# Kernel tuning notes

Hardware: AMD Instinct MI355X
Metric: run time of the kernel (lower is better)

Reference implementation:

```python
import jax, jax.numpy as jnp
import numpy as np

N, E, IN, H, OUT = 100000, 1600000, 64, 64, 10
NEG_SLOPE = 0.2  # PyG GATConv default negative_slope


def _glorot(key, shape):
    fan = sum(shape) if len(shape) > 1 else shape[0]
    return jax.random.normal(key, shape, dtype=jnp.float32) * jnp.sqrt(2.0 / fan)


def setup_inputs() -> dict:
    key = jax.random.key(0)
    ks = jax.random.split(key, 16)
    x = jax.random.normal(ks[0], (N, IN), dtype=jnp.float32)
    edge_index = jax.random.randint(ks[1], (2, E), 0, N, dtype=jnp.int32)
    dims = [(IN, H), (H, H), (H, OUT)]
    params = {}
    for i, (fi, fo) in enumerate(dims, start=1):
        params[f"W{i}"] = _glorot(ks[4 * i - 2], (fi, fo))
        params[f"a{i}s"] = _glorot(ks[4 * i - 1], (fo,))
        params[f"a{i}d"] = _glorot(ks[4 * i], (fo,))
        params[f"b{i}"] = jnp.zeros((fo,), dtype=jnp.float32)
    return {"x": x, "edge_index": edge_index, **params}


def gat_conv(x, src, dst, W, a_s, a_d, b):
    """Single-head GATConv (PyG defaults): gather -> leaky_relu scores ->
    segment softmax over dst -> scatter-add aggregate."""
    n = x.shape[0]
    h = x @ W                                   # [N, Fo]
    alpha_src = h @ a_s                          # [N]
    alpha_dst = h @ a_d                          # [N]
    e = jax.nn.leaky_relu(alpha_src[src] + alpha_dst[dst], NEG_SLOPE)  # [E']
    m = jax.ops.segment_max(e, dst, num_segments=n)                    # stable softmax max
    ex = jnp.exp(e - m[dst])
    denom = jax.ops.segment_sum(ex, dst, num_segments=n)
    alpha = ex / denom[dst]                      # [E'] per-dst softmax
    out = jax.ops.segment_sum(alpha[:, None] * h[src], dst, num_segments=n)
    return out + b


def reference(x, edge_index, W1, a1s, a1d, b1, W2, a2s, a2d, b2, W3, a3s, a3d, b3):
    n = x.shape[0]
    loops = jnp.arange(n, dtype=edge_index.dtype)  # add_self_loops=True
    src = jnp.concatenate([edge_index[0], loops])
    dst = jnp.concatenate([edge_index[1], loops])
    h = jax.nn.relu(gat_conv(x, src, dst, W1, a1s, a1d, b1))
    # dropout is identity at inference (training=False)
    h = jax.nn.relu(gat_conv(h, src, dst, W2, a2s, a2d, b2))
    h = gat_conv(h, src, dst, W3, a3s, a3d, b3)
    return jax.nn.log_softmax(h, axis=1)
```

## Files before the change

### kernel.cpp

```cpp
#include <hip/hip_runtime.h>
#include <math.h>
#include <type_traits>


#define NEG_SLOPE 0.2f
#define BKT_BITS 9
#define BKT_SZ   512
#define PACK_SRC_BITS 20

typedef _Float16 h8v __attribute__((ext_vector_type(8)));
typedef _Float16 h4v __attribute__((ext_vector_type(4)));
typedef float f4v __attribute__((ext_vector_type(4)));

__global__ __launch_bounds__(512) void k_bscan(const int* __restrict__ bcount, int nb,
                                               int E, int N, int* __restrict__ ebase,
                                               int* __restrict__ gcur,
                                               int* __restrict__ rowptr) {
    __shared__ int sm[BKT_SZ];
    int t = threadIdx.x;
    int v = (t < nb) ? bcount[t] : 0;
    sm[t] = v;
    __syncthreads();
    for (int o = 1; o < BKT_SZ; o <<= 1) {
        int tv = (t >= o) ? sm[t - o] : 0;
        __syncthreads();
        sm[t] += tv;
        __syncthreads();
    }
    int excl = sm[t] - v;
    if (t < nb) {
        ebase[t] = excl;
        gcur[t] = excl;
    }
    if (t == nb - 1) ebase[nb] = excl + v;
    if (t == 0) rowptr[N] = E + N;
}

__global__ __launch_bounds__(1024) void k_bscatter(const int* __restrict__ src,
                                                   const int* __restrict__ dst, int E,
                                                   int nb, int* __restrict__ gcur,
                                                   int* __restrict__ ebuf) {
    __shared__ int lc[BKT_SZ];
    __shared__ int gb[BKT_SZ];
    for (int i = threadIdx.x; i < nb; i += 1024) lc[i] = 0;
    __syncthreads();
    int base = blockIdx.x * 8192;
    int bkt[8], rnk[8], pk[8];
#pragma unroll
    for (int j = 0; j < 8; j++) {
        int i = base + j * 1024 + threadIdx.x;
        bkt[j] = -1;
        if (i < E) {
            int d = dst[i];
            int s = src[i];
            int b = d >> BKT_BITS;
            bkt[j] = b;
            rnk[j] = atomicAdd(&lc[b], 1);
            pk[j] = ((d & (BKT_SZ - 1)) << PACK_SRC_BITS) | s;
        }
    }
    __syncthreads();
    for (int b = threadIdx.x; b < nb; b += 1024)
        if (lc[b]) gb[b] = atomicAdd(&gcur[b], lc[b]);
    __syncthreads();
#pragma unroll
    for (int j = 0; j < 8; j++)
        if (bkt[j] >= 0) ebuf[gb[bkt[j]] + rnk[j]] = pk[j];
}

__global__ __launch_bounds__(512) void k_bcsr(const int* __restrict__ ebuf,
                                              const int* __restrict__ ebase, int N,
                                              int* __restrict__ rowptr,
                                              int* __restrict__ csr) {
    __shared__ int cnt[BKT_SZ];
    __shared__ int sm[BKT_SZ];
    int b = blockIdx.x;
    int t = threadIdx.x;
    int n0 = b << BKT_BITS;
    int nn = min(BKT_SZ, N - n0);
    cnt[t] = 0;
    __syncthreads();
    int e0 = ebase[b], e1 = ebase[b + 1];
    for (int i = e0 + t; i < e1; i += BKT_SZ)
        atomicAdd(&cnt[ebuf[i] >> PACK_SRC_BITS], 1);
    __syncthreads();
    int v = cnt[t] + (t < nn ? 1 : 0);
    sm[t] = v;
    __syncthreads();
    for (int o = 1; o < BKT_SZ; o <<= 1) {
        int tv = (t >= o) ? sm[t - o] : 0;
        __syncthreads();
        sm[t] += tv;
        __syncthreads();
    }
    int excl = sm[t] - v;
    int cb = e0 + n0;
    if (t < nn) {
        rowptr[n0 + t] = cb + excl;
        csr[cb + excl] = n0 + t;
    }
    cnt[t] = excl + 1;
    __syncthreads();
    for (int i = e0 + t; i < e1; i += BKT_SZ) {
        int p = ebuf[i];
        int dl = p >> PACK_SRC_BITS;
        int pos = atomicAdd(&cnt[dl], 1);
        csr[cb + pos] = p & ((1 << PACK_SRC_BITS) - 1);
    }
}

__global__ __launch_bounds__(256) void k_fill(const int* __restrict__ csr,
                                              const float* __restrict__ asb,
                                              int Etot, float* __restrict__ asbE) {
    int tid = blockIdx.x * 256 + threadIdx.x;
    int nth = gridDim.x * 256;
    int i = tid;
    for (; i + 3 * nth < Etot; i += 4 * nth) {
        int s0 = csr[i];
        int s1 = csr[i + nth];
        int s2 = csr[i + 2 * nth];
        int s3 = csr[i + 3 * nth];
        float v0 = asb[s0];
        float v1 = asb[s1];
        float v2 = asb[s2];
        float v3 = asb[s3];
        asbE[i] = v0;
        asbE[i + nth] = v1;
        asbE[i + 2 * nth] = v2;
        asbE[i + 3 * nth] = v3;
    }
    for (; i < Etot; i += nth) asbE[i] = asb[csr[i]];
}

__device__ __forceinline__ void gemm64_body(
    int bid, int nblocks, const float* __restrict__ X, const float* __restrict__ W,
    const float* __restrict__ a_s, const float* __restrict__ a_d, int N,
    _Float16* __restrict__ H, float* __restrict__ asb, float* __restrict__ adb) {
    constexpr int NT = 4;
    int lane = threadIdx.x & 63;
    int quad = lane >> 4;
    int c16 = lane & 15;

    h8v bf[NT][2];
    float asv[NT], adv[NT];
#pragma unroll
    for (int nt = 0; nt < NT; nt++) {
        int n = nt * 16 + c16;
        asv[nt] = a_s[n];
        adv[nt] = a_d[n];
#pragma unroll
        for (int kt = 0; kt < 2; kt++)
#pragma unroll
            for (int j = 0; j < 8; j++) {
                int k = kt * 32 + quad * 8 + j;
                bf[nt][kt][j] = (_Float16)W[k * 64 + n];
            }
    }

    int wid = (bid * 256 + (int)threadIdx.x) >> 6;
    int nw = (nblocks * 256) >> 6;
    int ntile = (N + 15) >> 4;

    for (int t = wid; t < ntile; t += nw) {
        int m0 = t << 4;
        int row = m0 + c16;
        const float* xr = X + (size_t)min(row, N - 1) * 64;
        h8v af[2];
#pragma unroll
        for (int kt = 0; kt < 2; kt++) {
            f4v x0 = *(const f4v*)(xr + kt * 32 + quad * 8);
            f4v x1 = *(const f4v*)(xr + kt * 32 + quad * 8 + 4);
#pragma unroll
            for (int j = 0; j < 4; j++) {
                af[kt][j] = (_Float16)x0[j];
                af[kt][4 + j] = (_Float16)x1[j];
            }
        }
        f4v c[NT];
#pragma unroll
        for (int nt = 0; nt < NT; nt++) c[nt] = (f4v){0.f, 0.f, 0.f, 0.f};
#pragma unroll
        for (int kt = 0; kt < 2; kt++)
#pragma unroll
            for (int nt = 0; nt < NT; nt++)
                c[nt] = __builtin_amdgcn_mfma_f32_16x16x32_f16(af[kt], bf[nt][kt],
                                                               c[nt], 0, 0, 0);
#pragma unroll
        for (int reg = 0; reg < 4; reg++) {
            int r = m0 + quad * 4 + reg;
            if (r < N) {
#pragma unroll
                for (int nt = 0; nt < NT; nt++)
                    H[(size_t)r * 64 + nt * 16 + c16] = (_Float16)c[nt][reg];
            }
        }
        float ps[4], pd[4];
#pragma unroll
        for (int reg = 0; reg < 4; reg++) {
            ps[reg] = 0.f;
            pd[reg] = 0.f;
#pragma unroll
            for (int nt = 0; nt < NT; nt++) {
                ps[reg] = fmaf(c[nt][reg], asv[nt], ps[reg]);
                pd[reg] = fmaf(c[nt][reg], adv[nt], pd[reg]);
            }
        }
        for (int o = 1; o < 16; o <<= 1) {
#pragma unroll
            for (int reg = 0; reg < 4; reg++) {
                ps[reg] += __shfl_xor(ps[reg], o, 64);
                pd[reg] += __shfl_xor(pd[reg], o, 64);
            }
        }
        if (c16 == 0) {
#pragma unroll
            for (int reg = 0; reg < 4; reg++) {
                int r = m0 + quad * 4 + reg;
                if (r < N) {
                    asb[r] = ps[reg];
                    adb[r] = pd[reg];
                }
            }
        }
    }
}

__global__ __launch_bounds__(256) void k_hist_gemm(
    const int* __restrict__ dst, int E, int nb, int* __restrict__ bcount,
    int histBlocks,
    const float* __restrict__ X, const float* __restrict__ W,
    const float* __restrict__ a_s, const float* __restrict__ a_d, int N,
    _Float16* __restrict__ H, float* __restrict__ asb, float* __restrict__ adb) {
    __shared__ int h[BKT_SZ];
    int bid = blockIdx.x;
    if (bid < histBlocks) {
        for (int i = threadIdx.x; i < nb; i += 256) h[i] = 0;
        __syncthreads();
        for (int i = bid * 256 + threadIdx.x; i < E; i += histBlocks * 256)
            atomicAdd(&h[dst[i] >> BKT_BITS], 1);
        __syncthreads();
        for (int i = threadIdx.x; i < nb; i += 256)
            if (h[i]) atomicAdd(&bcount[i], h[i]);
    } else {
        gemm64_body(bid - histBlocks, (int)gridDim.x - histBlocks, X, W, a_s, a_d,
                    N, H, asb, adb);
    }
}

template <int FP, typename InT>
__global__ __launch_bounds__(256) void k_gemm(
    const InT* __restrict__ X, const float* __restrict__ W,
    const float* __restrict__ a_s, const float* __restrict__ a_d,
    int N, int Freal,
    _Float16* __restrict__ H, float* __restrict__ asb, float* __restrict__ adb) {
    constexpr int NT = FP / 16;
    int lane = threadIdx.x & 63;
    int quad = lane >> 4;
    int c16 = lane & 15;

    h8v bf[NT][2];
    float asv[NT], adv[NT];
#pragma unroll
    for (int nt = 0; nt < NT; nt++) {
        int n = nt * 16 + c16;
        bool ok = (n < Freal);
        asv[nt] = ok ? a_s[n] : 0.f;
        adv[nt] = ok ? a_d[n] : 0.f;
#pragma unroll
        for (int kt = 0; kt < 2; kt++)
#pragma unroll
            for (int j = 0; j < 8; j++) {
                int k = kt * 32 + quad * 8 + j;
                bf[nt][kt][j] = (_Float16)(ok ? W[k * Freal + n] : 0.f);
            }
    }

    int wid = (blockIdx.x * blockDim.x + threadIdx.x) >> 6;
    int nw = (gridDim.x * blockDim.x) >> 6;
    int ntile = (N + 15) >> 4;

    for (int t = wid; t < ntile; t += nw) {
        int m0 = t << 4;
        int row = m0 + c16;
        const InT* xr = X + (size_t)min(row, N - 1) * 64;
        h8v af[2];
        if constexpr (std::is_same<InT, float>::value) {
#pragma unroll
            for (int kt = 0; kt < 2; kt++) {
                f4v x0 = *(const f4v*)(xr + kt * 32 + quad * 8);
                f4v x1 = *(const f4v*)(xr + kt * 32 + quad * 8 + 4);
#pragma unroll
                for (int j = 0; j < 4; j++) {
                    af[kt][j] = (_Float16)x0[j];
                    af[kt][4 + j] = (_Float16)x1[j];
                }
            }
        } else {
#pragma unroll
            for (int kt = 0; kt < 2; kt++)
                af[kt] = *(const h8v*)(xr + kt * 32 + quad * 8);
        }
        f4v c[NT];
#pragma unroll
        for (int nt = 0; nt < NT; nt++) c[nt] = (f4v){0.f, 0.f, 0.f, 0.f};
#pragma unroll
        for (int kt = 0; kt < 2; kt++)
#pragma unroll
            for (int nt = 0; nt < NT; nt++)
                c[nt] = __builtin_amdgcn_mfma_f32_16x16x32_f16(af[kt], bf[nt][kt],
                                                               c[nt], 0, 0, 0);
#pragma unroll
        for (int reg = 0; reg < 4; reg++) {
            int r = m0 + quad * 4 + reg;
            if (r < N) {
#pragma unroll
                for (int nt = 0; nt < NT; nt++)
                    H[(size_t)r * FP + nt * 16 + c16] = (_Float16)c[nt][reg];
            }
        }
        float ps[4], pd[4];
#pragma unroll
        for (int reg = 0; reg < 4; reg++) {
            ps[reg] = 0.f;
            pd[reg] = 0.f;
#pragma unroll
            for (int nt = 0; nt < NT; nt++) {
                ps[reg] = fmaf(c[nt][reg], asv[nt], ps[reg]);
                pd[reg] = fmaf(c[nt][reg], adv[nt], pd[reg]);
            }
        }
        for (int o = 1; o < 16; o <<= 1) {
#pragma unroll
            for (int reg = 0; reg < 4; reg++) {
                ps[reg] += __shfl_xor(ps[reg], o, 64);
                pd[reg] += __shfl_xor(pd[reg], o, 64);
            }
        }
        if (c16 == 0) {
#pragma unroll
            for (int reg = 0; reg < 4; reg++) {
                int r = m0 + quad * 4 + reg;
                if (r < N) {
                    asb[r] = ps[reg];
                    adb[r] = pd[reg];
                }
            }
        }
    }
}

template <int FP>
__device__ __forceinline__ void agg_slow(
    int node, const _Float16* __restrict__ H, const float* __restrict__ asbE,
    const float* __restrict__ adb, const float* __restrict__ bias,
    const int* __restrict__ rowptr, const int* __restrict__ csr,
    int N, int Freal, void* __restrict__ out, int mode, int lane) {
    if (node >= N) return;
    int start = rowptr[node];
    int end = rowptr[node + 1];
    float ad = adb[node];
    int lf = lane & (FP - 1);
    const float NEG_INF = -__builtin_inff();

    float m = NEG_INF;
    for (int base = start; base < end; base += 64) {
        int i = base + lane;
        if (i < end) {
            float t = asbE[i] + ad;
            float e = (t > 0.f) ? t : NEG_SLOPE * t;
            m = fmaxf(m, e);
        }
    }
    for (int o = 32; o > 0; o >>= 1) m = fmaxf(m, __shfl_xor(m, o, 64));
    float dsum = 0.f, acc = 0.f;
    for (int base = start; base < end; base += 64) {
        int i = base + lane;
        int cnt = min(64, end - base);
        int s = 0;
        float p = 0.f;
        if (i < end) {
            s = csr[i];
            float t = asbE[i] + ad;
            float e = (t > 0.f) ? t : NEG_SLOPE * t;
            p = __expf(e - m);
        }
        dsum += p;
        for (int j = 0; j < cnt; j++) {
            float pj = __shfl(p, j, 64);
            int sj = __shfl(s, j, 64);
            acc = fmaf(pj, (float)H[(size_t)sj * FP + lf], acc);
        }
    }
    for (int o = 32; o > 0; o >>= 1) dsum += __shfl_xor(dsum, o, 64);

    float b = (lf < Freal) ? bias[lf] : 0.f;
    float z = acc / dsum + b;
    if (mode == 0) {
        if (lane < FP)
            ((_Float16*)out)[(size_t)node * FP + lane] = (_Float16)fmaxf(z, 0.f);
    } else {
        float zz = (lane < Freal) ? z : NEG_INF;
        float zm = zz;
        for (int o = 32; o > 0; o >>= 1) zm = fmaxf(zm, __shfl_xor(zm, o, 64));
        float ez = (lane < Freal) ? __expf(zz - zm) : 0.f;
        float es = ez;
        for (int o = 32; o > 0; o >>= 1) es += __shfl_xor(es, o, 64);
        if (lane < Freal)
            ((float*)out)[(size_t)node * Freal + lane] = zz - zm - __logf(es);
    }
}

template <int FP, int W>
__global__ __launch_bounds__(256) void k_agg(
    const _Float16* __restrict__ H, const float* __restrict__ asbE,
    const float* __restrict__ adb, const float* __restrict__ bias,
    const int* __restrict__ rowptr, const int* __restrict__ csr,
    int N, int Freal, void* __restrict__ out, int mode) {
    constexpr int LPR = FP / W;
    constexpr int GRPH = 32 / LPR;
    constexpr int MAXIT = 32 / GRPH;
    using vecW = typename std::conditional<W == 8, h8v, h4v>::type;
    int lane = threadIdx.x & 63;
    int half = lane >> 5;
    int li = lane & 31;
    int wid = (blockIdx.x * blockDim.x + threadIdx.x) >> 6;
    int nA = 2 * wid;
    if (nA >= N) return;
    int n = nA + half;
    bool valid = (n < N);
    int start = 0, end = 0;
    float ad = 0.f;
    if (valid) {
        start = rowptr[n];
        end = rowptr[n + 1];
        ad = adb[n];
    }
    int deg = end - start;
    int degm = max(deg, __shfl_xor(deg, 32, 64));

    const float NEG_INF = -__builtin_inff();

    if (degm <= 32) {
        int g = li / LPR;
        int fl = li % LPR;
        bool have = (li < deg);
        int s = 0;
        float as_v = 0.f;
        if (have) {
            s = csr[start + li];
            as_v = asbE[start + li];
        }

        vecW r[MAXIT];
        int gidx = half * 32 + g;
#pragma unroll
        for (int it = 0; it < MAXIT; ++it) {
            if (it * GRPH < degm) {
                int sj = __shfl(s, gidx + it * GRPH, 64);
                r[it] = ((const vecW*)(H + (size_t)sj * FP))[fl];
            }
        }

        float e = NEG_INF;
        if (have) {
            float t = as_v + ad;
            e = (t > 0.f) ? t : NEG_SLOPE * t;
        }
        float m = e;
        for (int o = 16; o > 0; o >>= 1) m = fmaxf(m, __shfl_xor(m, o, 64));
        float p = have ? __expf(e - m) : 0.f;

        float acc[W];
#pragma unroll
        for (int c = 0; c < W; c++) acc[c] = 0.f;
#pragma unroll
        for (int it = 0; it < MAXIT; ++it) {
            if (it * GRPH < degm) {
                float pj = __shfl(p, gidx + it * GRPH, 64);
#pragma unroll
                for (int c = 0; c < W; c++)
                    acc[c] = fmaf(pj, (float)r[it][c], acc[c]);
            }
        }

        float dsum = p;
        for (int o = 16; o > 0; o >>= 1) dsum += __shfl_xor(dsum, o, 64);

        for (int o = LPR; o < 32; o <<= 1) {
#pragma unroll
            for (int c = 0; c < W; c++) acc[c] += __shfl_xor(acc[c], o, 64);
        }
        float inv = 1.f / dsum;
        int fbase = fl * W;

        if (mode == 0) {
            if (valid && li < LPR) {
                vecW zh;
#pragma unroll
                for (int c = 0; c < W; c++)
                    zh[c] = (_Float16)fmaxf(fmaf(acc[c], inv, bias[fbase + c]), 0.f);
                ((vecW*)((_Float16*)out + (size_t)n * FP))[fl] = zh;
            }
        } else {
            float zc[W];
#pragma unroll
            for (int c = 0; c < W; c++) {
                int f = fbase + c;
                zc[c] = (f < Freal) ? fmaf(acc[c], inv, bias[f]) : NEG_INF;
            }
            float vm = zc[0];
#pragma unroll
            for (int c = 1; c < W; c++) vm = fmaxf(vm, zc[c]);
            for (int o = 1; o < LPR; o <<= 1) vm = fmaxf(vm, __shfl_xor(vm, o, 64));
            float es = 0.f;
#pragma unroll
            for (int c = 0; c < W; c++) es += __expf(zc[c] - vm);
            for (int o = 1; o < LPR; o <<= 1) es += __shfl_xor(es, o, 64);
            float ls = __logf(es);
            if (valid && li < LPR) {
#pragma unroll
                for (int c = 0; c < W; c++) {
                    int f = fbase + c;
                    if (f < Freal)
                        ((float*)out)[(size_t)n * Freal + f] = zc[c] - vm - ls;
                }
            }
        }
    } else {
        agg_slow<FP>(nA, H, asbE, adb, bias, rowptr, csr, N, Freal, out, mode, lane);
        agg_slow<FP>(nA + 1, H, asbE, adb, bias, rowptr, csr, N, Freal, out, mode, lane);
    }
}

extern "C" void kernel_launch(void* const* d_in, const int* in_sizes, int n_in,
                              void* d_out, int out_size, void* d_ws, size_t ws_size,
                              hipStream_t stream) {
    const float* x = (const float*)d_in[0];
    const int* ei = (const int*)d_in[1];
    const float* W1 = (const float*)d_in[2];
    const float* a1s = (const float*)d_in[3];
    const float* a1d = (const float*)d_in[4];
    const float* b1 = (const float*)d_in[5];
    const float* W2 = (const float*)d_in[6];
    const float* a2s = (const float*)d_in[7];
    const float* a2d = (const float*)d_in[8];
    const float* b2 = (const float*)d_in[9];
    const float* W3 = (const float*)d_in[10];
    const float* a3s = (const float*)d_in[11];
    const float* a3d = (const float*)d_in[12];
    const float* b3 = (const float*)d_in[13];

    const int N = in_sizes[0] / 64;
    const int E = in_sizes[1] / 2;
    const int Etot = E + N;
    const int nb = (N + BKT_SZ - 1) >> BKT_BITS;
    const int* srcv = ei;
    const int* dstv = ei + E;

    size_t off = 0;
    char* base = (char*)d_ws;
    auto carve = [&](size_t bytes) -> void* {
        void* p = base + off;
        off = (off + bytes + 255) & ~(size_t)255;
        return p;
    };
    int* bcount = (int*)carve((size_t)(nb + 1) * 4);
    int* ebase = (int*)carve((size_t)(nb + 1) * 4);
    int* gcur = (int*)carve((size_t)nb * 4);
    int* rowptr = (int*)carve((size_t)(N + 1) * 4);
    int* csr = (int*)carve((size_t)Etot * 4);
    float* asb = (float*)carve((size_t)N * 4);
    float* adb = (float*)carve((size_t)N * 4);
    float* asbE = (float*)carve((size_t)Etot * 4);
    _Float16* hA = (_Float16*)carve((size_t)N * 64 * 2);
    _Float16* fB = (_Float16*)carve((size_t)N * 64 * 2);
    _Float16* hC = (_Float16*)carve((size_t)N * 16 * 2);
    int* ebuf = (int*)carve((size_t)E * 4);

    const int aggBlocks = (N + 7) / 8;
    const int gemmBlocks = 784;
    const int histBlocks = 512;
    const int fillBlocks = 1024;

    hipMemsetAsync(bcount, 0, (size_t)nb * 4, stream);
    k_hist_gemm<<<histBlocks + gemmBlocks, 256, 0, stream>>>(
        dstv, E, nb, bcount, histBlocks, x, W1, a1s, a1d, N, hA, asb, adb);
    k_bscan<<<1, BKT_SZ, 0, stream>>>(bcount, nb, E, N, ebase, gcur, rowptr);
    k_bscatter<<<(E + 8191) / 8192, 1024, 0, stream>>>(srcv, dstv, E, nb, gcur, ebuf);
    k_bcsr<<<nb, BKT_SZ, 0, stream>>>(ebuf, ebase, N, rowptr, csr);

    k_fill<<<fillBlocks, 256, 0, stream>>>(csr, asb, Etot, asbE);
    k_agg<64, 8><<<aggBlocks, 256, 0, stream>>>(hA, asbE, adb, b1, rowptr, csr, N, 64,
                                                (void*)fB, 0);
    k_gemm<64, _Float16><<<gemmBlocks, 256, 0, stream>>>(fB, W2, a2s, a2d, N, 64, hA,
                                                         asb, adb);
    k_fill<<<fillBlocks, 256, 0, stream>>>(csr, asb, Etot, asbE);
    k_agg<64, 8><<<aggBlocks, 256, 0, stream>>>(hA, asbE, adb, b2, rowptr, csr, N, 64,
                                                (void*)fB, 0);
    k_gemm<16, _Float16><<<gemmBlocks, 256, 0, stream>>>(fB, W3, a3s, a3d, N, 10, hC,
                                                         asb, adb);
    k_fill<<<fillBlocks, 256, 0, stream>>>(csr, asb, Etot, asbE);
    k_agg<16, 4><<<aggBlocks, 256, 0, stream>>>(hC, asbE, adb, b3, rowptr, csr, N, 10,
                                                d_out, 1);
}
```

Measured before the change: 332.2 us.

## Fold attention projections into aggregation epilogue and fuse fill with GEMM/CSR build

Precomputes W·a_s and W·a_d for layers 2 and 3 so the next layer's per-node attention logits come straight from the aggregation output, which removes that reduction from the GEMM. The layer-1 source-score gather now happens while the CSR is built, which drops one fill kernel. The other fills run as extra blocks inside the GEMM launch so both share one grid. This cuts three launches and overlaps a gather-bound pass with MFMA work, at the cost of extra shuffles in the aggregation epilogue and slightly different rounding, since the logits are computed from the fp32 pre-GEMM activations.

```diff
diff --git a/kernel.cpp b/kernel.cpp
--- a/kernel.cpp
+++ b/kernel.cpp
@@ -12,12 +12,34 @@
 typedef _Float16 h4v __attribute__((ext_vector_type(4)));
 typedef float f4v __attribute__((ext_vector_type(4)));
 
-__global__ __launch_bounds__(512) void k_bscan(const int* __restrict__ bcount, int nb,
-                                               int E, int N, int* __restrict__ ebase,
-                                               int* __restrict__ gcur,
-                                               int* __restrict__ rowptr) {
+__global__ __launch_bounds__(512) void k_bscan(
+    const int* __restrict__ bcount, int nb, int E, int N,
+    int* __restrict__ ebase, int* __restrict__ gcur, int* __restrict__ rowptr,
+    const float* __restrict__ W2, const float* __restrict__ a2s,
+    const float* __restrict__ a2d, const float* __restrict__ W3,
+    const float* __restrict__ a3s, const float* __restrict__ a3d,
+    float* __restrict__ w2s, float* __restrict__ w2d,
+    float* __restrict__ w3s, float* __restrict__ w3d) {
     __shared__ int sm[BKT_SZ];
     int t = threadIdx.x;
+
+    if (t < 64) {
+        float s2 = 0.f, d2 = 0.f;
+        for (int k = 0; k < 64; k++) {
+            s2 = fmaf(W2[t * 64 + k], a2s[k], s2);
+            d2 = fmaf(W2[t * 64 + k], a2d[k], d2);
+        }
+        w2s[t] = s2;
+        w2d[t] = d2;
+        float s3 = 0.f, d3 = 0.f;
+        for (int k = 0; k < 10; k++) {
+            s3 = fmaf(W3[t * 10 + k], a3s[k], s3);
+            d3 = fmaf(W3[t * 10 + k], a3d[k], d3);
+        }
+        w3s[t] = s3;
+        w3d[t] = d3;
+    }
+
     int v = (t < nb) ? bcount[t] : 0;
     sm[t] = v;
     __syncthreads();
@@ -71,7 +93,9 @@
 __global__ __launch_bounds__(512) void k_bcsr(const int* __restrict__ ebuf,
                                               const int* __restrict__ ebase, int N,
                                               int* __restrict__ rowptr,
-                                              int* __restrict__ csr) {
+                                              int* __restrict__ csr,
+                                              const float* __restrict__ asb,
+                                              float* __restrict__ asbE) {
     __shared__ int cnt[BKT_SZ];
     __shared__ int sm[BKT_SZ];
     int b = blockIdx.x;
@@ -98,38 +122,19 @@
     if (t < nn) {
         rowptr[n0 + t] = cb + excl;
         csr[cb + excl] = n0 + t;
+        asbE[cb + excl] = asb[n0 + t];
     }
     cnt[t] = excl + 1;
     __syncthreads();
     for (int i = e0 + t; i < e1; i += BKT_SZ) {
         int p = ebuf[i];
+        int s = p & ((1 << PACK_SRC_BITS) - 1);
+        float vv = asb[s];
         int dl = p >> PACK_SRC_BITS;
         int pos = atomicAdd(&cnt[dl], 1);
-        csr[cb + pos] = p & ((1 << PACK_SRC_BITS) - 1);
-    }
-}
-
-__global__ __launch_bounds__(256) void k_fill(const int* __restrict__ csr,
-                                              const float* __restrict__ asb,
-                                              int Etot, float* __restrict__ asbE) {
-    int tid = blockIdx.x * 256 + threadIdx.x;
-    int nth = gridDim.x * 256;
-    int i = tid;
-    for (; i + 3 * nth < Etot; i += 4 * nth) {
-        int s0 = csr[i];
-        int s1 = csr[i + nth];
-        int s2 = csr[i + 2 * nth];
-        int s3 = csr[i + 3 * nth];
-        float v0 = asb[s0];
-        float v1 = asb[s1];
-        float v2 = asb[s2];
-        float v3 = asb[s3];
-        asbE[i] = v0;
-        asbE[i + nth] = v1;
-        asbE[i + 2 * nth] = v2;
-        asbE[i + 3 * nth] = v3;
-    }
-    for (; i < Etot; i += nth) asbE[i] = asb[csr[i]];
+        csr[cb + pos] = s;
+        asbE[cb + pos] = vv;
+    }
 }
 
 __device__ __forceinline__ void gemm64_body(
@@ -247,25 +252,20 @@
     }
 }
 
-template <int FP, typename InT>
-__global__ __launch_bounds__(256) void k_gemm(
-    const InT* __restrict__ X, const float* __restrict__ W,
-    const float* __restrict__ a_s, const float* __restrict__ a_d,
-    int N, int Freal,
-    _Float16* __restrict__ H, float* __restrict__ asb, float* __restrict__ adb) {
+template <int FP>
+__device__ __forceinline__ void gemm_body(
+    int bid, int nblocks, const _Float16* __restrict__ X,
+    const float* __restrict__ W, int N, int Freal, _Float16* __restrict__ H) {
     constexpr int NT = FP / 16;
     int lane = threadIdx.x & 63;
     int quad = lane >> 4;
     int c16 = lane & 15;
 
     h8v bf[NT][2];
-    float asv[NT], adv[NT];
 #pragma unroll
     for (int nt = 0; nt < NT; nt++) {
         int n = nt * 16 + c16;
         bool ok = (n < Freal);
-        asv[nt] = ok ? a_s[n] : 0.f;
-        adv[nt] = ok ? a_d[n] : 0.f;
 #pragma unroll
         for (int kt = 0; kt < 2; kt++)
 #pragma unroll
@@ -275,31 +275,18 @@
             }
     }
 
-    int wid = (blockIdx.x * blockDim.x + threadIdx.x) >> 6;
-    int nw = (gridDim.x * blockDim.x) >> 6;
+    int wid = (bid * 256 + (int)threadIdx.x) >> 6;
+    int nw = (nblocks * 256) >> 6;
     int ntile = (N + 15) >> 4;
 
     for (int t = wid; t < ntile; t += nw) {
         int m0 = t << 4;
         int row = m0 + c16;
-        const InT* xr = X + (size_t)min(row, N - 1) * 64;
+        const _Float16* xr = X + (size_t)min(row, N - 1) * 64;
         h8v af[2];
-        if constexpr (std::is_same<InT, float>::value) {
-#pragma unroll
-            for (int kt = 0; kt < 2; kt++) {
-                f4v x0 = *(const f4v*)(xr + kt * 32 + quad * 8);
-                f4v x1 = *(const f4v*)(xr + kt * 32 + quad * 8 + 4);
-#pragma unroll
-                for (int j = 0; j < 4; j++) {
-                    af[kt][j] = (_Float16)x0[j];
-                    af[kt][4 + j] = (_Float16)x1[j];
-                }
-            }
-        } else {
-#pragma unroll
-            for (int kt = 0; kt < 2; kt++)
-                af[kt] = *(const h8v*)(xr + kt * 32 + quad * 8);
-        }
+#pragma unroll
+        for (int kt = 0; kt < 2; kt++)
+            af[kt] = *(const h8v*)(xr + kt * 32 + quad * 8);
         f4v c[NT];
 #pragma unroll
         for (int nt = 0; nt < NT; nt++) c[nt] = (f4v){0.f, 0.f, 0.f, 0.f};
@@ -318,34 +305,37 @@
                     H[(size_t)r * FP + nt * 16 + c16] = (_Float16)c[nt][reg];
             }
         }
-        float ps[4], pd[4];
-#pragma unroll
-        for (int reg = 0; reg < 4; reg++) {
-            ps[reg] = 0.f;
-            pd[reg] = 0.f;
-#pragma unroll
-            for (int nt = 0; nt < NT; nt++) {
-                ps[reg] = fmaf(c[nt][reg], asv[nt], ps[reg]);
-                pd[reg] = fmaf(c[nt][reg], adv[nt], pd[reg]);
-            }
-        }
-        for (int o = 1; o < 16; o <<= 1) {
-#pragma unroll
-            for (int reg = 0; reg < 4; reg++) {
-                ps[reg] += __shfl_xor(ps[reg], o, 64);
-                pd[reg] += __shfl_xor(pd[reg], o, 64);
-            }
-        }
-        if (c16 == 0) {
-#pragma unroll
-            for (int reg = 0; reg < 4; reg++) {
-                int r = m0 + quad * 4 + reg;
-                if (r < N) {
-                    asb[r] = ps[reg];
-                    adb[r] = pd[reg];
-                }
-            }
-        }
+    }
+}
+
+template <int FP>
+__global__ __launch_bounds__(256) void k_gemm_fill(
+    const _Float16* __restrict__ X, const float* __restrict__ W, int N, int Freal,
+    _Float16* __restrict__ H,
+    const int* __restrict__ csr, const float* __restrict__ asbN, int Etot,
+    float* __restrict__ asbE, int fillBlocks) {
+    int bid = blockIdx.x;
+    if (bid < fillBlocks) {
+        int nth = fillBlocks * 256;
+        int i = bid * 256 + threadIdx.x;
+        for (; i + 3 * nth < Etot; i += 4 * nth) {
+            int s0 = csr[i];
+            int s1 = csr[i + nth];
+            int s2 = csr[i + 2 * nth];
+            int s3 = csr[i + 3 * nth];
+            float v0 = asbN[s0];
+            float v1 = asbN[s1];
+            float v2 = asbN[s2];
+            float v3 = asbN[s3];
+            asbE[i] = v0;
+            asbE[i + nth] = v1;
+            asbE[i + 2 * nth] = v2;
+            asbE[i + 3 * nth] = v3;
+        }
+        for (; i < Etot; i += nth) asbE[i] = asbN[csr[i]];
+    } else {
+        gemm_body<FP>(bid - fillBlocks, (int)gridDim.x - fillBlocks, X, W, N,
+                      Freal, H);
     }
 }
 
@@ -354,7 +344,9 @@
     int node, const _Float16* __restrict__ H, const float* __restrict__ asbE,
     const float* __restrict__ adb, const float* __restrict__ bias,
     const int* __restrict__ rowptr, const int* __restrict__ csr,
-    int N, int Freal, void* __restrict__ out, int mode, int lane) {
+    int N, int Freal, void* __restrict__ out, int mode, int lane,
+    const float* __restrict__ wns, const float* __restrict__ wnd,
+    float* __restrict__ asbN, float* __restrict__ adbN) {
     if (node >= N) return;
     int start = rowptr[node];
     int end = rowptr[node + 1];
@@ -396,8 +388,21 @@
     float b = (lf < Freal) ? bias[lf] : 0.f;
     float z = acc / dsum + b;
     if (mode == 0) {
+        float zr = fmaxf(z, 0.f);
         if (lane < FP)
-            ((_Float16*)out)[(size_t)node * FP + lane] = (_Float16)fmaxf(z, 0.f);
+            ((_Float16*)out)[(size_t)node * FP + lane] = (_Float16)zr;
+        if (wns) {
+            float ps = zr * wns[lf];
+            float pd = zr * wnd[lf];
+            for (int o = 32; o > 0; o >>= 1) {
+                ps += __shfl_xor(ps, o, 64);
+                pd += __shfl_xor(pd, o, 64);
+            }
+            if (lane == 0) {
+                asbN[node] = ps;
+                adbN[node] = pd;
+            }
+        }
     } else {
         float zz = (lane < Freal) ? z : NEG_INF;
         float zm = zz;
@@ -415,7 +420,9 @@
     const _Float16* __restrict__ H, const float* __restrict__ asbE,
     const float* __restrict__ adb, const float* __restrict__ bias,
     const int* __restrict__ rowptr, const int* __restrict__ csr,
-    int N, int Freal, void* __restrict__ out, int mode) {
+    int N, int Freal, void* __restrict__ out, int mode,
+    const float* __restrict__ wns, const float* __restrict__ wnd,
+    float* __restrict__ asbN, float* __restrict__ adbN) {
     constexpr int LPR = FP / W;
     constexpr int GRPH = 32 / LPR;
     constexpr int MAXIT = 32 / GRPH;
@@ -494,12 +501,31 @@
         int fbase = fl * W;
 
         if (mode == 0) {
+            float z[W];
+#pragma unroll
+            for (int c = 0; c < W; c++)
+                z[c] = fmaxf(fmaf(acc[c], inv, bias[fbase + c]), 0.f);
             if (valid && li < LPR) {
                 vecW zh;
 #pragma unroll
-                for (int c = 0; c < W; c++)
-                    zh[c] = (_Float16)fmaxf(fmaf(acc[c], inv, bias[fbase + c]), 0.f);
+                for (int c = 0; c < W; c++) zh[c] = (_Float16)z[c];
                 ((vecW*)((_Float16*)out + (size_t)n * FP))[fl] = zh;
+            }
+            if (wns) {
+                float ps = 0.f, pd = 0.f;
+#pragma unroll
+                for (int c = 0; c < W; c++) {
+                    ps = fmaf(z[c], wns[fbase + c], ps);
+                    pd = fmaf(z[c], wnd[fbase + c], pd);
+                }
+                for (int o = 1; o < LPR; o <<= 1) {
+                    ps += __shfl_xor(ps, o, 64);
+                    pd += __shfl_xor(pd, o, 64);
+                }
+                if (valid && li == 0) {
+                    asbN[n] = ps;
+                    adbN[n] = pd;
+                }
             }
         } else {
             float zc[W];
@@ -527,8 +553,10 @@
             }
         }
     } else {
-        agg_slow<FP>(nA, H, asbE, adb, bias, rowptr, csr, N, Freal, out, mode, lane);
-        agg_slow<FP>(nA + 1, H, asbE, adb, bias, rowptr, csr, N, Freal, out, mode, lane);
+        agg_slow<FP>(nA, H, asbE, adb, bias, rowptr, csr, N, Freal, out, mode,
+                     lane, wns, wnd, asbN, adbN);
+        agg_slow<FP>(nA + 1, H, asbE, adb, bias, rowptr, csr, N, Freal, out, mode,
+                     lane, wns, wnd, asbN, adbN);
     }
 }
 
@@ -569,9 +597,15 @@
     int* gcur = (int*)carve((size_t)nb * 4);
     int* rowptr = (int*)carve((size_t)(N + 1) * 4);
     int* csr = (int*)carve((size_t)Etot * 4);
-    float* asb = (float*)carve((size_t)N * 4);
-    float* adb = (float*)carve((size_t)N * 4);
+    float* asb1 = (float*)carve((size_t)N * 4);
+    float* adb1 = (float*)carve((size_t)N * 4);
+    float* asb2 = (float*)carve((size_t)N * 4);
+    float* adb2 = (float*)carve((size_t)N * 4);
     float* asbE = (float*)carve((size_t)Etot * 4);
+    float* w2s = (float*)carve(64 * 4);
+    float* w2d = (float*)carve(64 * 4);
+    float* w3s = (float*)carve(64 * 4);
+    float* w3d = (float*)carve(64 * 4);
     _Float16* hA = (_Float16*)carve((size_t)N * 64 * 2);
     _Float16* fB = (_Float16*)carve((size_t)N * 64 * 2);
     _Float16* hC = (_Float16*)carve((size_t)N * 16 * 2);
@@ -580,26 +614,28 @@
     const int aggBlocks = (N + 7) / 8;
     const int gemmBlocks = 784;
     const int histBlocks = 512;
-    const int fillBlocks = 1024;
+    const int fillBlocks = 512;
 
     hipMemsetAsync(bcount, 0, (size_t)nb * 4, stream);
     k_hist_gemm<<<histBlocks + gemmBlocks, 256, 0, stream>>>(
-        dstv, E, nb, bcount, histBlocks, x, W1, a1s, a1d, N, hA, asb, adb);
-    k_bscan<<<1, BKT_SZ, 0, stream>>>(bcount, nb, E, N, ebase, gcur, rowptr);
+        dstv, E, nb, bcount, histBlocks, x, W1, a1s, a1d, N, hA, asb1, adb1);
+    k_bscan<<<1, BKT_SZ, 0, stream>>>(bcount, nb, E, N, ebase, gcur, rowptr,
+                                      W2, a2s, a2d, W3, a3s, a3d,
+                                      w2s, w2d, w3s, w3d);
     k_bscatter<<<(E + 8191) / 8192, 1024, 0, stream>>>(srcv, dstv, E, nb, gcur, ebuf);
-    k_bcsr<<<nb, BKT_SZ, 0, stream>>>(ebuf, ebase, N, rowptr, csr);
-
-    k_fill<<<fillBlocks, 256, 0, stream>>>(csr, asb, Etot, asbE);
-    k_agg<64, 8><<<aggBlocks, 256, 0, stream>>>(hA, asbE, adb, b1, rowptr, csr, N, 64,
-                                                (void*)fB, 0);
-    k_gemm<64, _Float16><<<gemmBlocks, 256, 0, stream>>>(fB, W2, a2s, a2d, N, 64, hA,
-                                                         asb, adb);
-    k_fill<<<fillBlocks, 256, 0, stream>>>(csr, asb, Etot, asbE);
-    k_agg<64, 8><<<aggBlocks, 256, 0, stream>>>(hA, asbE, adb, b2, rowptr, csr, N, 64,
-                                                (void*)fB, 0);
-    k_gemm<16, _Float16><<<gemmBlocks, 256, 0, stream>>>(fB, W3, a3s, a3d, N, 10, hC,
-                                                         asb, adb);
-    k_fill<<<fillBlocks, 256, 0, stream>>>(csr, asb, Etot, asbE);
-    k_agg<16, 4><<<aggBlocks, 256, 0, stream>>>(hC, asbE, adb, b3, rowptr, csr, N, 10,
-                                                d_out, 1);
-}
+    k_bcsr<<<nb, BKT_SZ, 0, stream>>>(ebuf, ebase, N, rowptr, csr, asb1, asbE);
+
+    k_agg<64, 8><<<aggBlocks, 256, 0, stream>>>(hA, asbE, adb1, b1, rowptr, csr,
+                                                N, 64, (void*)fB, 0,
+                                                w2s, w2d, asb2, adb2);
+    k_gemm_fill<64><<<fillBlocks + gemmBlocks, 256, 0, stream>>>(
+        fB, W2, N, 64, hA, csr, asb2, Etot, asbE, fillBlocks);
+    k_agg<64, 8><<<aggBlocks, 256, 0, stream>>>(hA, asbE, adb2, b2, rowptr, csr,
+                                                N, 64, (void*)fB, 0,
+                                                w3s, w3d, asb1, adb1);
+    k_gemm_fill<16><<<fillBlocks + gemmBlocks, 256, 0, stream>>>(
+        fB, W3, N, 10, hC, csr, asb1, Etot, asbE, fillBlocks);
+    k_agg<16, 4><<<aggBlocks, 256, 0, stream>>>(hC, asbE, adb1, b3, rowptr, csr,
+                                                N, 10, d_out, 1,
+                                                nullptr, nullptr, nullptr, nullptr);
+}
```

Result: no change. 337.9 us (+1.7%).
